# Kernel optimization log

Measured on AMD Instinct MI355X. Metric: run time of the kernel, lower is better.

## Reference

```python
import jax, jax.numpy as jnp
import numpy as np

NEG_INF = -1e38


def _wkv_scan(time_decay, time_first, key, value):
    # key, value: [B, S, D]; time_decay/time_first: [D]
    B, S, D = key.shape
    w = -jnp.exp(time_decay)  # decay applied additively in log-space

    def step(carry, kv):
        num, den, mx = carry
        k, v = kv  # [B, D]
        # output with current token boosted by time_first
        m_out = jnp.maximum(mx, k + time_first)
        e1 = jnp.exp(mx - m_out)
        e2 = jnp.exp(k + time_first - m_out)
        out = (e1 * num + e2 * v) / (e1 * den + e2)
        # state update with decay
        m_new = jnp.maximum(mx + w, k)
        e1 = jnp.exp(mx + w - m_new)
        e2 = jnp.exp(k - m_new)
        return (e1 * num + e2 * v, e1 * den + e2, m_new), out

    init = (jnp.zeros((B, D), jnp.float32),
            jnp.zeros((B, D), jnp.float32),
            jnp.full((B, D), NEG_INF, jnp.float32))
    kv = (jnp.moveaxis(key, 1, 0), jnp.moveaxis(value, 1, 0))  # [S, B, D]
    _, out = jax.lax.scan(step, init, kv)
    return jnp.moveaxis(out, 0, 1)  # [B, S, D]


def setup_inputs() -> dict:
    key = jax.random.key(0)
    ks = jax.random.split(key, 10)
    B, S, H = 4, 2048, 2048
    D = H  # attention_hidden_size
    return {
        "hidden": jax.random.normal(ks[0], (B, S, H), jnp.float32),
        "time_decay": jax.random.normal(ks[1], (D,), jnp.float32),
        "time_first": jax.random.normal(ks[2], (D,), jnp.float32),
        "time_mix_key": jax.random.uniform(ks[3], (1, 1, H), jnp.float32),
        "time_mix_value": jax.random.uniform(ks[4], (1, 1, H), jnp.float32),
        "time_mix_receptance": jax.random.uniform(ks[5], (1, 1, H), jnp.float32),
        "Wk": jax.random.normal(ks[6], (D, H), jnp.float32) / np.sqrt(H),  # torch Linear weight [out, in]
        "Wv": jax.random.normal(ks[7], (D, H), jnp.float32) / np.sqrt(H),
        "Wr": jax.random.normal(ks[8], (D, H), jnp.float32) / np.sqrt(H),
        "Wo": jax.random.normal(ks[9], (H, D), jnp.float32) / np.sqrt(D),
    }


def reference(hidden, time_decay, time_first, time_mix_key, time_mix_value,
              time_mix_receptance, Wk, Wv, Wr, Wo):
    # time_shift: prepend a zero timestep, drop the last (ZeroPad2d((0,0,1,-1)))
    shifted = jnp.pad(hidden, ((0, 0), (1, 0), (0, 0)))[:, :-1]
    xk = hidden * time_mix_key + shifted * (1.0 - time_mix_key)
    xv = hidden * time_mix_value + shifted * (1.0 - time_mix_value)
    xr = hidden * time_mix_receptance + shifted * (1.0 - time_mix_receptance)
    k = jnp.einsum('bsh,dh->bsd', xk, Wk)
    v = jnp.einsum('bsh,dh->bsd', xv, Wv)
    r = jax.nn.sigmoid(jnp.einsum('bsh,dh->bsd', xr, Wr))
    rwkv = _wkv_scan(time_decay, time_first, k, v)
    return jnp.einsum('bsd,hd->bsh', r * rwkv, Wo)
```

## Files before the change

### kernel.cpp

```cpp
#include <hip/hip_runtime.h>


typedef __attribute__((ext_vector_type(8))) short s16x8;
typedef __attribute__((ext_vector_type(16))) float f32x16;

__device__ __forceinline__ unsigned short f2bf(float f) {
  union { float f; unsigned u; } v; v.f = f;
  unsigned r = v.u + 0x7fffu + ((v.u >> 16) & 1u);
  return (unsigned short)(r >> 16);
}
__device__ __forceinline__ float bf2f(unsigned short h) {
  union { unsigned u; float f; } v; v.u = ((unsigned)h) << 16; return v.f;
}
__device__ __forceinline__ void gload_lds16(const void* g, void* l) {
  __builtin_amdgcn_global_load_lds(
      (const __attribute__((address_space(1))) void*)g,
      (__attribute__((address_space(3))) void*)l, 16, 0, 0);
}


__global__ void conv_bf16(const float4* __restrict__ src, ushort4* __restrict__ dst, int n4) {
  int i = blockIdx.x * blockDim.x + threadIdx.x;
  if (i >= n4) return;
  float4 v = src[i];
  ushort4 o;
  o.x = f2bf(v.x); o.y = f2bf(v.y); o.z = f2bf(v.z); o.w = f2bf(v.w);
  dst[i] = o;
}


__global__ void prep_mix3(const float4* __restrict__ hidden,
                          const float4* __restrict__ tmk,
                          const float4* __restrict__ tmv,
                          const float4* __restrict__ tmr,
                          ushort4* __restrict__ xk, ushort4* __restrict__ xv,
                          ushort4* __restrict__ xr,
                          int S, int H4, long long total4) {
  long long i = (long long)blockIdx.x * blockDim.x + threadIdx.x;
  if (i >= total4) return;
  int h4 = (int)(i % H4);
  long long sb = i / H4;
  int s = (int)(sb % S);
  float4 cur = hidden[i];
  float4 prev = make_float4(0.f, 0.f, 0.f, 0.f);
  if (s > 0) prev = hidden[i - H4];
  float4 mk = tmk[h4], mv = tmv[h4], mr = tmr[h4];
  ushort4 ok, ov, orr;
  ok.x = f2bf(cur.x * mk.x + prev.x * (1.f - mk.x));
  ok.y = f2bf(cur.y * mk.y + prev.y * (1.f - mk.y));
  ok.z = f2bf(cur.z * mk.z + prev.z * (1.f - mk.z));
  ok.w = f2bf(cur.w * mk.w + prev.w * (1.f - mk.w));
  ov.x = f2bf(cur.x * mv.x + prev.x * (1.f - mv.x));
  ov.y = f2bf(cur.y * mv.y + prev.y * (1.f - mv.y));
  ov.z = f2bf(cur.z * mv.z + prev.z * (1.f - mv.z));
  ov.w = f2bf(cur.w * mv.w + prev.w * (1.f - mv.w));
  orr.x = f2bf(cur.x * mr.x + prev.x * (1.f - mr.x));
  orr.y = f2bf(cur.y * mr.y + prev.y * (1.f - mr.y));
  orr.z = f2bf(cur.z * mr.z + prev.z * (1.f - mr.z));
  orr.w = f2bf(cur.w * mr.w + prev.w * (1.f - mr.w));
  xk[i] = ok; xv[i] = ov; xr[i] = orr;
}


template <int EPI>
__global__ __launch_bounds__(512) void gemm_bt(
    const unsigned short* __restrict__ A, const unsigned short* __restrict__ B,
    float* __restrict__ Cf, unsigned short* __restrict__ Cb,
    int M, int N, int K) {
  __shared__ unsigned short lds[4][16384];

  const int tid = threadIdx.x;
  const int wave = tid >> 6;
  const int lane = tid & 63;

  const int nwg = (int)gridDim.x;
  const int q = nwg >> 3;
  const int wg = (blockIdx.x & 7) * q + (blockIdx.x >> 3);
  const int GM = M >> 8;
  const int bm = (wg % GM) * 256;
  const int bn = (wg / GM) * 256;

  const int wm = (wave >> 2) * 128;
  const int wn = (wave & 3) * 64;
  const int lrow = lane & 31;
  const int lq = lane >> 5;

  f32x16 acc[4][2] = {};

  const int srow = tid >> 2;
  const int sg = ((tid & 3) ^ ((srow >> 1) & 3)) * 8;
  const unsigned short* gA0 = A + (long long)(bm + srow) * K + sg;
  const unsigned short* gA1 = A + (long long)(bm + 128 + srow) * K + sg;
  const unsigned short* gB0 = B + (long long)(bn + srow) * K + sg;
  const unsigned short* gB1 = B + (long long)(bn + 128 + srow) * K + sg;

#define STAGE(sl)                                              \
  {                                                            \
    unsigned short* dst = &lds[sl][0] + wave * 512;            \
    gload_lds16(gA0, dst);                                     \
    gload_lds16(gA1, dst + 4096);                              \
    gload_lds16(gB0, dst + 8192);                              \
    gload_lds16(gB1, dst + 12288);                             \
    gA0 += 32; gA1 += 32; gB0 += 32; gB1 += 32;                \
  }

  int offA[4][2], offB[2][2];
#pragma unroll
  for (int mt = 0; mt < 4; ++mt)
#pragma unroll
    for (int h = 0; h < 2; ++h) {
      int R = wm + mt * 32 + lrow;
      int c = h * 2 + lq;
      offA[mt][h] = R * 32 + ((c ^ ((R >> 1) & 3)) * 8);
    }
#pragma unroll
  for (int nt = 0; nt < 2; ++nt)
#pragma unroll
    for (int h = 0; h < 2; ++h) {
      int Cc = wn + nt * 32 + lrow;
      int c = h * 2 + lq;
      offB[nt][h] = 8192 + Cc * 32 + ((c ^ ((Cc >> 1) & 3)) * 8);
    }

  const int NT = K >> 5;

  STAGE(0);
  STAGE(1);
  STAGE(2);
  asm volatile("s_waitcnt vmcnt(8)" ::: "memory");
  __builtin_amdgcn_sched_barrier(0);
  __builtin_amdgcn_s_barrier();

  for (int t = 0; t < NT; ++t) {
    const unsigned short* sb = &lds[t & 3][0];
    s16x8 af[4][2], bfr[2][2];
#pragma unroll
    for (int mt = 0; mt < 4; ++mt)
#pragma unroll
      for (int h = 0; h < 2; ++h)
        af[mt][h] = *(const s16x8*)(sb + offA[mt][h]);
#pragma unroll
    for (int nt = 0; nt < 2; ++nt)
#pragma unroll
      for (int h = 0; h < 2; ++h)
        bfr[nt][h] = *(const s16x8*)(sb + offB[nt][h]);

    if (t + 3 < NT) STAGE((t + 3) & 3);

    if (t + 3 < NT) {
      asm volatile("s_waitcnt vmcnt(8)" ::: "memory");
    } else if (t + 3 == NT) {
      asm volatile("s_waitcnt vmcnt(4)" ::: "memory");
    } else if (t + 2 == NT) {
      asm volatile("s_waitcnt vmcnt(0)" ::: "memory");
    }
    __builtin_amdgcn_sched_barrier(0);
    __builtin_amdgcn_s_barrier();

    __builtin_amdgcn_s_setprio(1);
#pragma unroll
    for (int h = 0; h < 2; ++h)
#pragma unroll
      for (int mt = 0; mt < 4; ++mt)
#pragma unroll
        for (int nt = 0; nt < 2; ++nt)
          acc[mt][nt] = __builtin_amdgcn_mfma_f32_32x32x16_bf16(
              af[mt][h], bfr[nt][h], acc[mt][nt], 0, 0, 0);
    __builtin_amdgcn_s_setprio(0);
    __builtin_amdgcn_s_barrier();
  }
#undef STAGE

#pragma unroll
  for (int mt = 0; mt < 4; ++mt)
#pragma unroll
    for (int nt = 0; nt < 2; ++nt)
#pragma unroll
      for (int r = 0; r < 16; ++r) {
        int row = bm + wm + mt * 32 + (r & 3) + 8 * (r >> 2) + 4 * lq;
        int col = bn + wn + nt * 32 + lrow;
        float v = acc[mt][nt][r];
        long long idx = (long long)row * N + col;
        if (EPI == 0) {
          Cf[idx] = v;
        } else if (EPI == 1) {
          float s = 1.f / (1.f + __expf(-v));
          Cb[idx] = f2bf(s);
        } else {
          Cb[idx] = f2bf(v);
        }
      }
}


#define NEG_INF_F (-1e38f)

__global__ void scan_phase1(const unsigned short* __restrict__ kb,
                            const unsigned short* __restrict__ vb,
                            const float* __restrict__ td,
                            float* __restrict__ locN, float* __restrict__ locD,
                            float* __restrict__ locM,
                            int S, int D, int C, int L) {
  int t = blockIdx.x * blockDim.x + threadIdx.x;
  int d = t % D;
  int c = (t / D) % C;
  int b = t / (D * C);
  float w = -__expf(td[d]);
  float num = 0.f, den = 0.f, m = NEG_INF_F;
  long long base = ((long long)(b * S + c * L)) * D + d;
  for (int i = 0; i < L; ++i) {
    float kk = bf2f(kb[base]);
    float vv = bf2f(vb[base]);
    base += D;
    float mn = fmaxf(m + w, kk);
    float e1 = __expf(m + w - mn);
    float e2 = __expf(kk - mn);
    num = e1 * num + e2 * vv;
    den = e1 * den + e2;
    m = mn;
  }
  int o = (b * C + c) * D + d;
  locN[o] = num; locD[o] = den; locM[o] = m;
}

__global__ void scan_phase2(const float* __restrict__ td,
                            const float* __restrict__ locN, const float* __restrict__ locD,
                            const float* __restrict__ locM,
                            float* __restrict__ inN, float* __restrict__ inD,
                            float* __restrict__ inM,
                            int Bc, int D, int C, int L) {
  int t = blockIdx.x * blockDim.x + threadIdx.x;
  if (t >= Bc * D) return;
  int d = t % D, b = t / D;
  float w = -__expf(td[d]);
  float Lw = (float)L * w;
  float num = 0.f, den = 0.f, m = NEG_INF_F;
  for (int c = 0; c < C; ++c) {
    int o = (b * C + c) * D + d;
    inN[o] = num; inD[o] = den; inM[o] = m;
    float sm = m + Lw;
    float lm = locM[o];
    float m2 = fmaxf(sm, lm);
    float e1 = __expf(sm - m2);
    float e2 = __expf(lm - m2);
    num = e1 * num + e2 * locN[o];
    den = e1 * den + e2 * locD[o];
    m = m2;
  }
}

__global__ void scan_phase3(const unsigned short* __restrict__ kb,
                            const unsigned short* __restrict__ vb,
                            const unsigned short* __restrict__ rb,
                            const float* __restrict__ td, const float* __restrict__ tfirst,
                            const float* __restrict__ inN, const float* __restrict__ inD,
                            const float* __restrict__ inM,
                            unsigned short* __restrict__ rr,
                            int S, int D, int C, int L) {
  int t = blockIdx.x * blockDim.x + threadIdx.x;
  int d = t % D;
  int c = (t / D) % C;
  int b = t / (D * C);
  float w = -__expf(td[d]);
  float tfd = tfirst[d];
  int o = (b * C + c) * D + d;
  float num = inN[o], den = inD[o], m = inM[o];
  long long base = ((long long)(b * S + c * L)) * D + d;
  for (int i = 0; i < L; ++i) {
    float kk = bf2f(kb[base]);
    float vv = bf2f(vb[base]);
    float rv = bf2f(rb[base]);
    float ktf = kk + tfd;
    float mo = fmaxf(m, ktf);
    float e1 = __expf(m - mo);
    float e2 = __expf(ktf - mo);
    float out = (e1 * num + e2 * vv) / (e1 * den + e2);
    rr[base] = f2bf(out * rv);
    float mn = fmaxf(m + w, kk);
    e1 = __expf(m + w - mn);
    e2 = __expf(kk - mn);
    num = e1 * num + e2 * vv;
    den = e1 * den + e2;
    m = mn;
    base += D;
  }
}


extern "C" void kernel_launch(void* const* d_in, const int* in_sizes, int n_in,
                              void* d_out, int out_size, void* d_ws, size_t ws_size,
                              hipStream_t stream) {
  const float* hidden = (const float*)d_in[0];
  const float* td  = (const float*)d_in[1];
  const float* tfi = (const float*)d_in[2];
  const float* tmk = (const float*)d_in[3];
  const float* tmv = (const float*)d_in[4];
  const float* tmr = (const float*)d_in[5];
  const float* Wk  = (const float*)d_in[6];
  const float* Wv  = (const float*)d_in[7];
  const float* Wr  = (const float*)d_in[8];
  const float* Wo  = (const float*)d_in[9];
  float* out = (float*)d_out;

  const int H = in_sizes[1];
  const int D = H;
  const long long BS = (long long)in_sizes[0] / H;
  const int S = 2048;
  const int B = (int)(BS / S);
  const int C = 32, L = S / C;

  char* ws = (char*)d_ws;
  const size_t MB = 1u << 20;
  unsigned short* W_b = (unsigned short*)(ws + 0 * MB);
  unsigned short* X   = (unsigned short*)(ws + 8 * MB);
  unsigned short* Y   = (unsigned short*)(ws + 40 * MB);
  unsigned short* Z   = (unsigned short*)(ws + 72 * MB);
  float* locN         = (float*)(ws + 104 * MB);
  float* locD         = (float*)(ws + 105 * MB);
  float* locM         = (float*)(ws + 106 * MB);
  float* inN          = (float*)(ws + 107 * MB);
  float* inD          = (float*)(ws + 108 * MB);
  float* inM          = (float*)(ws + 109 * MB);
  unsigned short* kb  = (unsigned short*)out;

  int n4w = H * H / 4;
  int cbk = (n4w + 255) / 256;
  long long total4 = BS * H / 4;
  int pbk = (int)((total4 + 255) / 256);
  int nwg = (int)((BS / 256) * (D / 256));

  prep_mix3<<<pbk, 256, 0, stream>>>((const float4*)hidden,
                                     (const float4*)tmk, (const float4*)tmv, (const float4*)tmr,
                                     (ushort4*)X, (ushort4*)Y, (ushort4*)Z, S, H / 4, total4);

  conv_bf16<<<cbk, 256, 0, stream>>>((const float4*)Wk, (ushort4*)W_b, n4w);
  gemm_bt<2><<<nwg, 512, 0, stream>>>(X, W_b, nullptr, kb, (int)BS, D, H);

  conv_bf16<<<cbk, 256, 0, stream>>>((const float4*)Wv, (ushort4*)W_b, n4w);
  gemm_bt<2><<<nwg, 512, 0, stream>>>(Y, W_b, nullptr, X, (int)BS, D, H);

  conv_bf16<<<cbk, 256, 0, stream>>>((const float4*)Wr, (ushort4*)W_b, n4w);
  gemm_bt<1><<<nwg, 512, 0, stream>>>(Z, W_b, nullptr, Y, (int)BS, D, H);

  int nscan = B * C * D;
  scan_phase1<<<nscan / 256, 256, 0, stream>>>(kb, X, td, locN, locD, locM, S, D, C, L);
  scan_phase2<<<(B * D + 255) / 256, 256, 0, stream>>>(td, locN, locD, locM, inN, inD, inM, B, D, C, L);
  scan_phase3<<<nscan / 256, 256, 0, stream>>>(kb, X, Y, td, tfi, inN, inD, inM, Z, S, D, C, L);

  conv_bf16<<<cbk, 256, 0, stream>>>((const float4*)Wo, (ushort4*)W_b, n4w);
  gemm_bt<0><<<nwg, 512, 0, stream>>>(Z, W_b, out, nullptr, (int)BS, H, D);
}
```

Baseline: 558.2 us.

## Split GEMM main loop into two phases interleaving A/B staging with MFMA halves

The bf16 GEMM main loop is split into two half-iterations. Each loads half of the A fragments, issues the prefetch of either the A or the B tile for a later stage, and runs half the MFMAs, with extra barriers between the halves. The aim is to interleave global-to-LDS loads and LDS reads with matrix-core work, and to lower register pressure by holding fewer A fragments at once. In exchange it adds barriers per iteration, which may add synchronization stalls.

```diff
diff --git a/kernel.cpp b/kernel.cpp
--- a/kernel.cpp
+++ b/kernel.cpp
@@ -94,14 +94,19 @@
   const unsigned short* gB0 = B + (long long)(bn + srow) * K + sg;
   const unsigned short* gB1 = B + (long long)(bn + 128 + srow) * K + sg;
 
-#define STAGE(sl)                                              \
+#define STAGE_A(sl)                                            \
   {                                                            \
     unsigned short* dst = &lds[sl][0] + wave * 512;            \
     gload_lds16(gA0, dst);                                     \
     gload_lds16(gA1, dst + 4096);                              \
+    gA0 += 32; gA1 += 32;                                      \
+  }
+#define STAGE_B(sl)                                            \
+  {                                                            \
+    unsigned short* dst = &lds[sl][0] + wave * 512;            \
     gload_lds16(gB0, dst + 8192);                              \
     gload_lds16(gB1, dst + 12288);                             \
-    gA0 += 32; gA1 += 32; gB0 += 32; gB1 += 32;                \
+    gB0 += 32; gB1 += 32;                                      \
   }
 
   int offA[4][2], offB[2][2];
@@ -124,18 +129,20 @@
 
   const int NT = K >> 5;
 
-  STAGE(0);
-  STAGE(1);
-  STAGE(2);
+  STAGE_A(0); STAGE_B(0);
+  STAGE_A(1); STAGE_B(1);
+  STAGE_A(2); STAGE_B(2);
   asm volatile("s_waitcnt vmcnt(8)" ::: "memory");
   __builtin_amdgcn_sched_barrier(0);
   __builtin_amdgcn_s_barrier();
 
   for (int t = 0; t < NT; ++t) {
     const unsigned short* sb = &lds[t & 3][0];
-    s16x8 af[4][2], bfr[2][2];
-#pragma unroll
-    for (int mt = 0; mt < 4; ++mt)
+    const bool pf = (t + 3 < NT);
+    s16x8 af[2][2], bfr[2][2];
+
+#pragma unroll
+    for (int mt = 0; mt < 2; ++mt)
 #pragma unroll
       for (int h = 0; h < 2; ++h)
         af[mt][h] = *(const s16x8*)(sb + offA[mt][h]);
@@ -145,9 +152,31 @@
       for (int h = 0; h < 2; ++h)
         bfr[nt][h] = *(const s16x8*)(sb + offB[nt][h]);
 
-    if (t + 3 < NT) STAGE((t + 3) & 3);
-
-    if (t + 3 < NT) {
+    if (pf) STAGE_A((t + 3) & 3);
+    __builtin_amdgcn_s_barrier();
+
+    __builtin_amdgcn_s_setprio(1);
+#pragma unroll
+    for (int h = 0; h < 2; ++h)
+#pragma unroll
+      for (int mt = 0; mt < 2; ++mt)
+#pragma unroll
+        for (int nt = 0; nt < 2; ++nt)
+          acc[mt][nt] = __builtin_amdgcn_mfma_f32_32x32x16_bf16(
+              af[mt][h], bfr[nt][h], acc[mt][nt], 0, 0, 0);
+    __builtin_amdgcn_s_setprio(0);
+    __builtin_amdgcn_s_barrier();
+
+    s16x8 ag[2][2];
+#pragma unroll
+    for (int mt = 0; mt < 2; ++mt)
+#pragma unroll
+      for (int h = 0; h < 2; ++h)
+        ag[mt][h] = *(const s16x8*)(sb + offA[2 + mt][h]);
+
+    if (pf) STAGE_B((t + 3) & 3);
+
+    if (pf) {
       asm volatile("s_waitcnt vmcnt(8)" ::: "memory");
     } else if (t + 3 == NT) {
       asm volatile("s_waitcnt vmcnt(4)" ::: "memory");
@@ -161,15 +190,16 @@
 #pragma unroll
     for (int h = 0; h < 2; ++h)
 #pragma unroll
-      for (int mt = 0; mt < 4; ++mt)
+      for (int mt = 0; mt < 2; ++mt)
 #pragma unroll
         for (int nt = 0; nt < 2; ++nt)
-          acc[mt][nt] = __builtin_amdgcn_mfma_f32_32x32x16_bf16(
-              af[mt][h], bfr[nt][h], acc[mt][nt], 0, 0, 0);
+          acc[2 + mt][nt] = __builtin_amdgcn_mfma_f32_32x32x16_bf16(
+              ag[mt][h], bfr[nt][h], acc[2 + mt][nt], 0, 0, 0);
     __builtin_amdgcn_s_setprio(0);
     __builtin_amdgcn_s_barrier();
   }
-#undef STAGE
+#undef STAGE_A
+#undef STAGE_B
 
 #pragma unroll
   for (int mt = 0; mt < 4; ++mt)
```

Result: no change. 554.9 us (-0.6%).
